# Kernel optimization log

Measured on AMD Instinct MI355X. Metric: run time of the kernel, lower is better.

## Reference

```python
import jax, jax.numpy as jnp
import numpy as np

B, N, D = 4, 2048, 1024
H, A, Lv = 8, 128, 128   # heads, attention_dim (qk), linear_dim (v)
NUM_BLOCKS = 4
QKV_W = (2 * Lv + 2 * A) * H  # 4096
NEG = -1e9


def setup_inputs() -> dict:
    key = jax.random.key(0)
    ks = jax.random.split(key, 10)
    past_lengths = jax.random.randint(ks[0], (B,), 0, N)
    past_ids = jax.random.randint(ks[1], (B, N), 0, 10000)
    past_embeddings = jax.random.normal(ks[2], (B, N, D), dtype=jnp.float32)
    # per-block parameters, stacked on leading block axis (xavier-ish scale)
    qkv_w = jax.random.normal(ks[3], (NUM_BLOCKS, D, QKV_W), dtype=jnp.float32) * (1.0 / np.sqrt(D))
    qkv_b = jnp.zeros((NUM_BLOCKS, QKV_W), dtype=jnp.float32)
    out_w = jax.random.normal(ks[4], (NUM_BLOCKS, Lv * H, D), dtype=jnp.float32) * (1.0 / np.sqrt(Lv * H))
    out_b = jnp.zeros((NUM_BLOCKS, D), dtype=jnp.float32)
    ln_g = jnp.ones((NUM_BLOCKS, D), dtype=jnp.float32)
    ln_b = jnp.zeros((NUM_BLOCKS, D), dtype=jnp.float32)
    return {"past_lengths": past_lengths, "past_ids": past_ids,
            "past_embeddings": past_embeddings, "qkv_w": qkv_w, "qkv_b": qkv_b,
            "out_w": out_w, "out_b": out_b, "ln_g": ln_g, "ln_b": ln_b}


def _layer_norm(x, g, b, eps=1e-5):
    mu = jnp.mean(x, axis=-1, keepdims=True)
    var = jnp.mean(jnp.square(x - mu), axis=-1, keepdims=True)
    return (x - mu) * jax.lax.rsqrt(var + eps) * g + b


def _block(x, mask, qw, qb, ow, ob, g, b):
    xn = _layer_norm(x, g, b)
    qkv = (xn @ qw + qb).reshape(B, N, H, 2 * Lv + 2 * A)
    q = qkv[..., :A]              # [B,N,H,A]
    k = qkv[..., A:2 * A]         # [B,N,H,A]
    v = qkv[..., 2 * A:2 * A + Lv]  # [B,N,H,Lv]
    scores = jnp.einsum('bnha,bmha->bhnm', q, k) / np.sqrt(A)
    # original: masked_fill(-inf) -> silu -> /N -> softmax; we mask after the
    # silu transform with a large-negative logit so masked weights are ~0
    logits = jnp.where(mask[:, None, :, :], jax.nn.silu(scores) / N, NEG)
    w = jax.nn.softmax(logits, axis=-1)
    attn = jnp.einsum('bhnm,bmhl->bnhl', w, v).reshape(B, N, H * Lv)
    return x + attn @ ow + ob


def reference(past_lengths, past_ids, past_embeddings, qkv_w, qkv_b, out_w, out_b, ln_g, ln_b):
    valid = past_ids != 0                                   # [B,N]
    causal = jnp.triu(jnp.ones((N, N), dtype=bool), k=1)     # faithful to buffer (triu, diag=1)
    mask = causal[None] & valid[:, None, :] & valid[:, :, None]  # [B,N,N]
    x = past_embeddings
    for i in range(NUM_BLOCKS):
        x = _block(x, mask, qkv_w[i], qkv_b[i], out_w[i], out_b[i], ln_g[i], ln_b[i])
    return x
```

## Files before the change

kernel.cpp:

```cpp
#include <hip/hip_runtime.h>

typedef __bf16 bf16_t;
typedef __bf16 bf16x8 __attribute__((ext_vector_type(8)));
typedef __bf16 bf16x4 __attribute__((ext_vector_type(4)));
typedef float f32x4 __attribute__((ext_vector_type(4)));

#define B_ 4
#define N_ 2048
#define D_ 1024
#define H_ 8
#define NB_ 4
#define M_ (B_*N_)
#define QN_ 3072
#define QKN_ 2048

__device__ __forceinline__ void async_copy16(const void* gsrc, void* ldst) {
    __builtin_amdgcn_global_load_lds(
        (const __attribute__((address_space(1))) void*)gsrc,
        (__attribute__((address_space(3))) void*)ldst, 16, 0, 0);
}

static constexpr size_t WT_OFF  = 0;
static constexpr size_t WT_SZ   = (size_t)NB_*QN_*D_*2;
static constexpr size_t OWT_OFF = WT_OFF + WT_SZ;
static constexpr size_t OWT_SZ  = (size_t)NB_*D_*D_*2;
static constexpr size_t XN_OFF  = OWT_OFF + OWT_SZ;
static constexpr size_t XN_SZ   = (size_t)M_*D_*2;
static constexpr size_t QK_OFF  = XN_OFF + XN_SZ;
static constexpr size_t QK_SZ   = (size_t)M_*QKN_*2;
static constexpr size_t VT_OFF  = QK_OFF + QK_SZ;
static constexpr size_t VT_SZ   = (size_t)32*128*N_*2;
static constexpr size_t ATT_OFF = VT_OFF + VT_SZ;
static constexpr size_t ATT_SZ  = (size_t)M_*D_*2;
static constexpr size_t QBR_OFF = ATT_OFF + ATT_SZ;
static constexpr size_t QBR_SZ  = (size_t)NB_*QN_*4;
static constexpr size_t VS_OFF  = QBR_OFF + QBR_SZ;

__global__ __launch_bounds__(256) void repack_qkvw(const float* __restrict__ qw, bf16_t* __restrict__ wt)
{
    __shared__ float tile[64][65];
    const int nb = blockIdx.z;
    const int j0 = blockIdx.x * 64, d0 = blockIdx.y * 64;
    const int tx = threadIdx.x, ty = threadIdx.y;
    const float* src = qw + (size_t)nb * D_ * 4096;
    const int jj = j0 + tx;
    const int sel = jj >> 10, rr = jj & 1023, hh = rr >> 7, aa = rr & 127;
    const int orig = hh * 512 + sel * 128 + aa;
#pragma unroll
    for (int it = 0; it < 16; ++it) {
        int dr = it * 4 + ty;
        tile[dr][tx] = src[(size_t)(d0 + dr) * 4096 + orig];
    }
    __syncthreads();
    bf16_t* dst = wt + (size_t)nb * QN_ * D_;
#pragma unroll
    for (int it = 0; it < 16; ++it) {
        int jr = it * 4 + ty;
        dst[(size_t)(j0 + jr) * D_ + d0 + tx] = (bf16_t)tile[tx][jr];
    }
}

__global__ __launch_bounds__(256) void repack_outw(const float* __restrict__ ow, bf16_t* __restrict__ owt)
{
    __shared__ float tile[64][65];
    const int nb = blockIdx.z;
    const int j0 = blockIdx.x * 64, d0 = blockIdx.y * 64;
    const int tx = threadIdx.x, ty = threadIdx.y;
    const float* src = ow + (size_t)nb * D_ * D_;
#pragma unroll
    for (int it = 0; it < 16; ++it) {
        int dr = it * 4 + ty;
        tile[dr][tx] = src[(size_t)(d0 + dr) * D_ + j0 + tx];
    }
    __syncthreads();
    bf16_t* dst = owt + (size_t)nb * D_ * D_;
#pragma unroll
    for (int it = 0; it < 16; ++it) {
        int jr = it * 4 + ty;
        dst[(size_t)(j0 + jr) * D_ + d0 + tx] = (bf16_t)tile[tx][jr];
    }
}

__global__ __launch_bounds__(256) void repack_qb(const float* __restrict__ qb, float* __restrict__ qbr)
{
    int idx = blockIdx.x * 256 + threadIdx.x;
    int nb = idx / QN_, jj = idx % QN_;
    int sel = jj >> 10, rr = jj & 1023, hh = rr >> 7, aa = rr & 127;
    qbr[idx] = qb[nb * 4096 + hh * 512 + sel * 128 + aa];
}

__global__ __launch_bounds__(256) void ln_kernel(const float* __restrict__ x, const float* __restrict__ g,
                                                 const float* __restrict__ bb, bf16_t* __restrict__ xn)
{
    const int row = blockIdx.x, tid = threadIdx.x;
    const float4 v = ((const float4*)(x + (size_t)row * D_))[tid];
    float s = v.x + v.y + v.z + v.w;
    float q = v.x * v.x + v.y * v.y + v.z * v.z + v.w * v.w;
#pragma unroll
    for (int d = 32; d >= 1; d >>= 1) { s += __shfl_xor(s, d); q += __shfl_xor(q, d); }
    __shared__ float ls[4], lq[4];
    if ((tid & 63) == 0) { ls[tid >> 6] = s; lq[tid >> 6] = q; }
    __syncthreads();
    s = ls[0] + ls[1] + ls[2] + ls[3];
    q = lq[0] + lq[1] + lq[2] + lq[3];
    const float mean = s * (1.f / 1024.f);
    const float var  = q * (1.f / 1024.f) - mean * mean;
    const float inv  = rsqrtf(var + 1e-5f);
    const float4 gg = ((const float4*)g)[tid];
    const float4 bv = ((const float4*)bb)[tid];
    bf16x4 o;
    o[0] = (bf16_t)((v.x - mean) * inv * gg.x + bv.x);
    o[1] = (bf16_t)((v.y - mean) * inv * gg.y + bv.y);
    o[2] = (bf16_t)((v.z - mean) * inv * gg.z + bv.z);
    o[3] = (bf16_t)((v.w - mean) * inv * gg.w + bv.w);
    *(bf16x4*)(xn + (size_t)row * D_ + tid * 4) = o;
}

__global__ __launch_bounds__(512, 2) void gemm_qkv(const bf16_t* __restrict__ Am, const bf16_t* __restrict__ Bt,
                                                   const float* __restrict__ bias,
                                                   bf16_t* __restrict__ outQK, bf16_t* __restrict__ vtOut)
{
    __shared__ bf16_t As[4 * 8192];
    __shared__ bf16_t Bs[4 * 6144];
    const int tid = threadIdx.x;
    const int lane = tid & 63, wave = tid >> 6;
    const int wr = wave >> 2, wc = wave & 3;
    const int quad = lane >> 4, l15 = lane & 15;
    const int swz = quad ^ ((l15 >> 1) & 3);
    const int slane8 = ((lane & 3) ^ ((lane >> 3) & 3)) * 8;
    const int lrow = lane >> 2;
    const int m0 = blockIdx.y * 256, n0 = blockIdx.x * 192;
    const int Kn = D_;
    const bool w4 = (wave < 4);

    const int ch = wave * 2;
    const int bch0 = w4 ? 2 * wave : 4 + wave;
    const int bch1 = w4 ? 2 * wave + 1 : bch0;
    const bf16_t* gA0 = Am + (size_t)(m0 + ch * 16 + lrow) * Kn + slane8;
    const bf16_t* gA1 = gA0 + (size_t)16 * Kn;
    const bf16_t* gB0 = Bt + (size_t)(n0 + bch0 * 16 + lrow) * Kn + slane8;
    const bf16_t* gB1 = Bt + (size_t)(n0 + bch1 * 16 + lrow) * Kn + slane8;
    bf16_t* const dA0 = &As[ch * 512 + lane * 8];
    bf16_t* const dA1 = &As[(ch + 1) * 512 + lane * 8];
    bf16_t* const dB0 = &Bs[bch0 * 512 + lane * 8];
    bf16_t* const dB1 = &Bs[bch1 * 512 + lane * 8];

    auto STAGE = [&](int slot) {
        async_copy16(gA0, dA0 + slot * 8192);
        async_copy16(gA1, dA1 + slot * 8192);
        async_copy16(gB0, dB0 + slot * 6144);
        if (w4) async_copy16(gB1, dB1 + slot * 6144);
        gA0 += 32; gA1 += 32; gB0 += 32; gB1 += 32;
    };

    f32x4 acc[8][3] = {};
    const int NT = Kn >> 5;

    STAGE(0); STAGE(1); STAGE(2);
    if (w4) asm volatile("s_waitcnt vmcnt(8)" ::: "memory");
    else    asm volatile("s_waitcnt vmcnt(6)" ::: "memory");
    __builtin_amdgcn_s_barrier();

    const int aoff = wr * 4096 + l15 * 32 + swz * 8;
    const int boff = wc * 1536 + l15 * 32 + swz * 8;

    for (int t = 0; t < NT; ++t) {
        const int ring = t & 3;
        const bf16_t* ra = &As[ring * 8192 + aoff];
        const bf16_t* rb = &Bs[ring * 6144 + boff];
        bf16x8 af[8], bfv[3];
#pragma unroll
        for (int j = 0; j < 3; ++j) bfv[j] = *(const bf16x8*)(rb + j * 512);
#pragma unroll
        for (int i = 0; i < 8; ++i) af[i] = *(const bf16x8*)(ra + i * 512);
        if (t + 3 < NT) STAGE((t + 3) & 3);
        __builtin_amdgcn_s_setprio(1);
#pragma unroll
        for (int i = 0; i < 8; ++i)
#pragma unroll
            for (int j = 0; j < 3; ++j)
                acc[i][j] = __builtin_amdgcn_mfma_f32_16x16x32_bf16(af[i], bfv[j], acc[i][j], 0, 0, 0);
        __builtin_amdgcn_s_setprio(0);
        if (t + 3 < NT) {
            if (w4) asm volatile("s_waitcnt vmcnt(8)" ::: "memory");
            else    asm volatile("s_waitcnt vmcnt(6)" ::: "memory");
        } else if (t + 2 < NT) {
            if (w4) asm volatile("s_waitcnt vmcnt(4)" ::: "memory");
            else    asm volatile("s_waitcnt vmcnt(3)" ::: "memory");
        } else if (t + 1 < NT) {
            asm volatile("s_waitcnt vmcnt(0)" ::: "memory");
        }
        __builtin_amdgcn_s_barrier();
    }

#pragma unroll
    for (int i = 0; i < 8; ++i) {
        const int rowg = m0 + wr * 128 + i * 16 + quad * 4;
        const int bb2 = rowg >> 11, mloc = rowg & 2047;
        const int mperm = (mloc & ~31) | (((mloc >> 2) & 3) << 3) | (((mloc >> 4) & 1) << 2);
#pragma unroll
        for (int j = 0; j < 3; ++j) {
            const int colg = n0 + wc * 48 + j * 16 + l15;
            const float bv = bias[colg];
            if (colg >= 2048) {
                const int hh = (colg - 2048) >> 7, ll = (colg - 2048) & 127;
                bf16x4 sv;
#pragma unroll
                for (int r = 0; r < 4; ++r) sv[r] = (bf16_t)(acc[i][j][r] + bv);
                *(bf16x4*)(vtOut + ((size_t)(bb2 * 8 + hh) * 128 + ll) * (size_t)N_ + mperm) = sv;
            } else {
#pragma unroll
                for (int r = 0; r < 4; ++r)
                    outQK[(size_t)(rowg + r) * QKN_ + colg] = (bf16_t)(acc[i][j][r] + bv);
            }
        }
    }
}

template<bool RESID>
__global__ __launch_bounds__(512, 2) void gemm256(const bf16_t* __restrict__ Am, const bf16_t* __restrict__ Bt,
                                                  const float* __restrict__ bias, float* __restrict__ resid_out,
                                                  bf16_t* __restrict__ outH, bf16_t* __restrict__ vtOut,
                                                  int Kn, int Nn, int vSplit)
{
    __shared__ bf16_t As[4 * 256 * 32];
    __shared__ bf16_t Bs[4 * 128 * 32];
    const int tid = threadIdx.x;
    const int lane = tid & 63, wave = tid >> 6;
    const int wr = wave >> 2, wc = wave & 3;
    const int quad = lane >> 4, l15 = lane & 15;
    const int swz = quad ^ ((l15 >> 1) & 3);
    const int slane8 = ((lane & 3) ^ ((lane >> 3) & 3)) * 8;
    const int lrow = lane >> 2;
    const int m0 = blockIdx.y * 256, n0 = blockIdx.x * 128;

    const int chA0 = wave * 2, chA1 = chA0 + 1;
    const bf16_t* gA0 = Am + (size_t)(m0 + chA0 * 16 + lrow) * Kn + slane8;
    const bf16_t* gA1 = Am + (size_t)(m0 + chA1 * 16 + lrow) * Kn + slane8;
    const bf16_t* gB  = Bt + (size_t)(n0 + wave * 16 + lrow) * Kn + slane8;
    bf16_t* const dA0 = &As[chA0 * 512];
    bf16_t* const dA1 = &As[chA1 * 512];
    bf16_t* const dB  = &Bs[wave * 512];

    auto STAGE = [&](int slot) {
        async_copy16(gA0, dA0 + slot * 8192);
        async_copy16(gA1, dA1 + slot * 8192);
        async_copy16(gB,  dB  + slot * 4096);
        gA0 += 32; gA1 += 32; gB += 32;
    };

    f32x4 acc[8][2] = {};
    const int NT = Kn >> 5;

    STAGE(0); STAGE(1); STAGE(2);
    asm volatile("s_waitcnt vmcnt(6)" ::: "memory");
    __builtin_amdgcn_s_barrier();

    const int aoff = (wr * 128 + l15) * 32 + swz * 8;
    const int boff = (wc * 32  + l15) * 32 + swz * 8;

    for (int t = 0; t < NT; ++t) {
        const int ring = t & 3;
        const bf16_t* ra = &As[ring * 8192 + aoff];
        const bf16_t* rb = &Bs[ring * 4096 + boff];
        bf16x8 af[8], bfv[2];
#pragma unroll
        for (int i = 0; i < 8; ++i) af[i] = *(const bf16x8*)(ra + i * 512);
#pragma unroll
        for (int j = 0; j < 2; ++j) bfv[j] = *(const bf16x8*)(rb + j * 512);
        if (t + 3 < NT) STAGE((t + 3) & 3);
        __builtin_amdgcn_s_barrier();
        asm volatile("s_waitcnt lgkmcnt(0)" ::: "memory");
        __builtin_amdgcn_s_setprio(1);
#pragma unroll
        for (int i = 0; i < 8; ++i)
#pragma unroll
            for (int j = 0; j < 2; ++j)
                acc[i][j] = __builtin_amdgcn_mfma_f32_16x16x32_bf16(af[i], bfv[j], acc[i][j], 0, 0, 0);
        __builtin_amdgcn_s_setprio(0);
        if (t + 3 < NT)      asm volatile("s_waitcnt vmcnt(6)" ::: "memory");
        else if (t + 2 < NT) asm volatile("s_waitcnt vmcnt(3)" ::: "memory");
        else if (t + 1 < NT) asm volatile("s_waitcnt vmcnt(0)" ::: "memory");
        __builtin_amdgcn_s_barrier();
    }

    if (!RESID && n0 >= vSplit) {
#pragma unroll
        for (int i = 0; i < 8; ++i) {
            const int rowg = m0 + wr * 128 + i * 16 + quad * 4;
            const int bb2 = rowg >> 11, mloc = rowg & 2047;
            const int mperm = (mloc & ~31) | (((mloc >> 2) & 3) << 3) | (((mloc >> 4) & 1) << 2);
#pragma unroll
            for (int j = 0; j < 2; ++j) {
                const int colg = n0 + wc * 32 + j * 16 + l15;
                const int hh = (colg - 2048) >> 7, ll = (colg - 2048) & 127;
                const float bv = bias[colg];
                bf16x4 sv;
#pragma unroll
                for (int r = 0; r < 4; ++r) sv[r] = (bf16_t)(acc[i][j][r] + bv);
                *(bf16x4*)(vtOut + ((size_t)(bb2 * 8 + hh) * 128 + ll) * (size_t)N_ + mperm) = sv;
            }
        }
        return;
    }
#pragma unroll
    for (int i = 0; i < 8; ++i) {
#pragma unroll
        for (int j = 0; j < 2; ++j) {
            const int colg = n0 + wc * 32 + j * 16 + l15;
            const float bv = bias[colg];
#pragma unroll
            for (int r = 0; r < 4; ++r) {
                const int rowg = m0 + wr * 128 + i * 16 + quad * 4 + r;
                const size_t off = (size_t)rowg * Nn + colg;
                const float v = acc[i][j][r] + bv;
                if (RESID) resid_out[off] += v;
                else       outH[off] = (bf16_t)v;
            }
        }
    }
}

__global__ __launch_bounds__(256) void vsum_kernel(const bf16_t* __restrict__ vt, float* __restrict__ vs)
{
    const int gid = blockIdx.x * 4 + (threadIdx.x >> 6);
    const int lane = threadIdx.x & 63;
    const bf16_t* p = vt + (size_t)gid * N_ + lane * 8;
    float s = 0.f;
#pragma unroll
    for (int c = 0; c < 4; ++c) {
        bf16x8 v = *(const bf16x8*)(p + c * 512);
#pragma unroll
        for (int u = 0; u < 8; ++u) s += (float)v[u];
    }
#pragma unroll
    for (int d = 32; d >= 1; d >>= 1) s += __shfl_xor(s, d);
    if (lane == 0) vs[gid] = s;
}

template<bool CAUSAL>
__device__ __forceinline__ void attn_tile(
    int m0, int m0n, int n0, int b, int h,
    const bf16_t* __restrict__ qk, const bf16_t* __restrict__ vtb,
    bf16_t* Ks, bf16_t* Vs, const unsigned int* mb,
    const bf16x8 (&qf)[2][4], bf16x8 onesf, float vnf0, float vnf1,
    f32x4 (&oacc)[2][8], f32x4 (&dacc)[2])
{
    const int tid = threadIdx.x, lane = tid & 63, wave = tid >> 6;
    const int quad = lane >> 4, l15 = lane & 15;
    const int swz = quad ^ ((l15 >> 1) & 3);
    const int slane8 = ((lane & 3) ^ ((lane >> 3) & 3)) * 8;
    const int lrow = lane >> 2;
    const float scaleA = 0.08838834764831845f;
    const float invN = 1.f / 2048.f;

#pragma unroll
    for (int s = 0; s < 8; ++s) {
        const int kkc = s & 3, rg = (s >> 2) + wave * 2;
        async_copy16(vtb + (size_t)(rg * 16 + lrow) * N_ + m0 + kkc * 32 + slane8,
                     &Vs[kkc * 4096 + rg * 512 + lane * 8]);
    }

    f32x4 sacc[2][8] = {};
    __builtin_amdgcn_s_setprio(1);
#pragma unroll
    for (int kk = 0; kk < 4; ++kk) {
#pragma unroll
        for (int j = 0; j < 8; ++j) {
            bf16x8 kf = *(const bf16x8*)&Ks[kk * 4096 + (j * 16 + l15) * 32 + swz * 8];
            sacc[0][j] = __builtin_amdgcn_mfma_f32_16x16x32_bf16(kf, qf[0][kk], sacc[0][j], 0, 0, 0);
            sacc[1][j] = __builtin_amdgcn_mfma_f32_16x16x32_bf16(kf, qf[1][kk], sacc[1][j], 0, 0, 0);
        }
    }
    __builtin_amdgcn_s_setprio(0);

    unsigned int wj[4];
#pragma unroll
    for (int q = 0; q < 4; ++q) wj[q] = mb[(m0 >> 5) + q];
    bf16x8 pf[2][4];
#pragma unroll
    for (int kk = 0; kk < 4; ++kk) {
#pragma unroll
        for (int s = 0; s < 2; ++s) {
            const int j = kk * 2 + s;
            const unsigned int wrd = wj[j >> 1];
            const int shl = (j & 1) * 16 + quad * 4;
#pragma unroll
            for (int nb = 0; nb < 2; ++nb) {
                const float vn = nb ? vnf1 : vnf0;
#pragma unroll
                for (int r = 0; r < 4; ++r) {
                    const float sv = sacc[nb][j][r] * scaleA;
                    const float xc = fminf(fmaxf(sv, -4.f), 4.f);
                    float sig = __builtin_fmaf(xc, 0.25f, 0.5f);
                    sig = __builtin_fmaf(-(xc * 0.03125f), fabsf(xc), sig);
                    float e = __builtin_fmaf(sv * sig, invN, 1.f);
                    e = ((wrd >> (shl + r)) & 1) ? e * vn : 0.f;
                    if (CAUSAL) {
                        const int dmn = (m0 + j * 16 + quad * 4 + r) - (n0 + wave * 32 + nb * 16 + l15);
                        e = (dmn > 0) ? e : 0.f;
                    }
                    pf[nb][kk][s * 4 + r] = (bf16_t)e;
                }
            }
        }
    }

    __syncthreads();

    if (m0n < N_) {
        const size_t baseq = (size_t)b * N_ * QKN_;
#pragma unroll
        for (int s = 0; s < 8; ++s) {
            const int kkc = s & 3, rg = (s >> 2) + wave * 2;
            async_copy16(qk + baseq + (size_t)(m0n + rg * 16 + lrow) * QKN_ + 1024 + h * 128 + kkc * 32 + slane8,
                         &Ks[kkc * 4096 + rg * 512 + lane * 8]);
        }
    }

    __builtin_amdgcn_s_setprio(1);
#pragma unroll
    for (int kk = 0; kk < 4; ++kk) {
        dacc[0] = __builtin_amdgcn_mfma_f32_16x16x32_bf16(pf[0][kk], onesf, dacc[0], 0, 0, 0);
        dacc[1] = __builtin_amdgcn_mfma_f32_16x16x32_bf16(pf[1][kk], onesf, dacc[1], 0, 0, 0);
#pragma unroll
        for (int j = 0; j < 8; ++j) {
            bf16x8 vf = *(const bf16x8*)&Vs[kk * 4096 + (j * 16 + l15) * 32 + swz * 8];
            oacc[0][j] = __builtin_amdgcn_mfma_f32_16x16x32_bf16(pf[0][kk], vf, oacc[0][j], 0, 0, 0);
            oacc[1][j] = __builtin_amdgcn_mfma_f32_16x16x32_bf16(pf[1][kk], vf, oacc[1][j], 0, 0, 0);
        }
    }
    __builtin_amdgcn_s_setprio(0);
    __syncthreads();
}

__global__ __launch_bounds__(256, 2) void attn_kernel(const bf16_t* __restrict__ qk, const bf16_t* __restrict__ vt,
                                                      const int* __restrict__ past_ids, const float* __restrict__ vsum,
                                                      bf16_t* __restrict__ att)
{
    __shared__ bf16_t Ks[4 * 128 * 32];
    __shared__ bf16_t Vs[4 * 128 * 32];
    __shared__ unsigned long long mbits[32];

    const int bx = blockIdx.x;
    const int bh = bx & 31, g = bx >> 5;
    const int t = (g < 8) ? g : 23 - g;
    const int b = bh >> 3, h = bh & 7;
    const int n0 = t << 7;
    const int tid = threadIdx.x, lane = tid & 63, wave = tid >> 6;
    const int quad = lane >> 4, l15 = lane & 15;
    const int slane8 = ((lane & 3) ^ ((lane >> 3) & 3)) * 8;
    const int lrow = lane >> 2;
    const bf16_t* vtb = vt + (size_t)bh * 128 * N_;
    const float invN = 1.f / 2048.f;

#pragma unroll
    for (int it = 0; it < 8; ++it) {
        const int m = (wave * 8 + it) * 64 + lane;
        const unsigned long long bal = __ballot(past_ids[b * N_ + m] != 0);
        if (lane == 0) mbits[wave * 8 + it] = bal;
    }

    bf16x8 qf[2][4];
#pragma unroll
    for (int nb = 0; nb < 2; ++nb) {
        const bf16_t* gq = qk + (size_t)b * N_ * QKN_ + (size_t)(n0 + wave * 32 + nb * 16 + l15) * QKN_ + h * 128 + quad * 8;
#pragma unroll
        for (int kk = 0; kk < 4; ++kk) qf[nb][kk] = *(const bf16x8*)(gq + kk * 32);
    }
    const float vnf0 = past_ids[b * N_ + n0 + wave * 32 + l15] != 0 ? 1.f : 0.f;
    const float vnf1 = past_ids[b * N_ + n0 + wave * 32 + 16 + l15] != 0 ? 1.f : 0.f;
    bf16x8 onesf;
#pragma unroll
    for (int i = 0; i < 8; ++i) onesf[i] = (bf16_t)1.f;

    {
        const size_t baseq = (size_t)b * N_ * QKN_;
#pragma unroll
        for (int s = 0; s < 8; ++s) {
            const int kkc = s & 3, rg = (s >> 2) + wave * 2;
            async_copy16(qk + baseq + (size_t)(n0 + rg * 16 + lrow) * QKN_ + 1024 + h * 128 + kkc * 32 + slane8,
                         &Ks[kkc * 4096 + rg * 512 + lane * 8]);
        }
    }
    __syncthreads();

    f32x4 oacc[2][8] = {};
    f32x4 dacc[2] = {};
    const unsigned int* mb = (const unsigned int*)mbits;

    attn_tile<true>(n0, n0 + 128, n0, b, h, qk, vtb, Ks, Vs, mb, qf, onesf, vnf0, vnf1, oacc, dacc);
    for (int m0 = n0 + 128; m0 < N_; m0 += 128)
        attn_tile<false>(m0, m0 + 128, n0, b, h, qk, vtb, Ks, Vs, mb, qf, onesf, vnf0, vnf1, oacc, dacc);

    float vsr[8];
#pragma unroll
    for (int j = 0; j < 8; ++j) vsr[j] = vsum[bh * 128 + j * 16 + l15];
#pragma unroll
    for (int nb = 0; nb < 2; ++nb) {
#pragma unroll
        for (int r = 0; r < 4; ++r) {
            const float dn = dacc[nb][r];
            const bool uni = !(dn > 0.f);
            const float rc = uni ? 0.f : __builtin_amdgcn_rcpf(dn);
            const int gn = n0 + wave * 32 + nb * 16 + quad * 4 + r;
#pragma unroll
            for (int j = 0; j < 8; ++j) {
                const float ov = uni ? (vsr[j] * invN) : (oacc[nb][j][r] * rc);
                att[(size_t)(b * N_ + gn) * 1024 + h * 128 + j * 16 + l15] = (bf16_t)ov;
            }
        }
    }
}

extern "C" void kernel_launch(void* const* d_in, const int* in_sizes, int n_in,
                              void* d_out, int out_size, void* d_ws, size_t ws_size,
                              hipStream_t stream) {
    (void)in_sizes; (void)n_in; (void)out_size; (void)ws_size;
    const int*   past_ids = (const int*)d_in[1];
    const float* past_emb = (const float*)d_in[2];
    const float* qkv_w    = (const float*)d_in[3];
    const float* qkv_b    = (const float*)d_in[4];
    const float* out_w    = (const float*)d_in[5];
    const float* out_b    = (const float*)d_in[6];
    const float* ln_g     = (const float*)d_in[7];
    const float* ln_b     = (const float*)d_in[8];

    float* x = (float*)d_out;
    char* ws = (char*)d_ws;
    bf16_t* WT  = (bf16_t*)(ws + WT_OFF);
    bf16_t* OWT = (bf16_t*)(ws + OWT_OFF);
    bf16_t* XN  = (bf16_t*)(ws + XN_OFF);
    bf16_t* QK  = (bf16_t*)(ws + QK_OFF);
    bf16_t* VT  = (bf16_t*)(ws + VT_OFF);
    bf16_t* ATT = (bf16_t*)(ws + ATT_OFF);
    float*  QBR = (float*)(ws + QBR_OFF);
    float*  VS  = (float*)(ws + VS_OFF);

    hipMemcpyAsync(x, past_emb, (size_t)M_ * D_ * sizeof(float), hipMemcpyDeviceToDevice, stream);
    repack_qkvw<<<dim3(48, 16, NB_), dim3(64, 4), 0, stream>>>(qkv_w, WT);
    repack_outw<<<dim3(16, 16, NB_), dim3(64, 4), 0, stream>>>(out_w, OWT);
    repack_qb<<<48, 256, 0, stream>>>(qkv_b, QBR);

    for (int layer = 0; layer < NB_; ++layer) {
        ln_kernel<<<M_, 256, 0, stream>>>(x, ln_g + layer * D_, ln_b + layer * D_, XN);
        gemm_qkv<<<dim3(QN_ / 192, M_ / 256), 512, 0, stream>>>(
            XN, WT + (size_t)layer * QN_ * D_, QBR + layer * QN_, QK, VT);
        vsum_kernel<<<1024, 256, 0, stream>>>(VT, VS);
        attn_kernel<<<512, 256, 0, stream>>>(QK, VT, past_ids, VS, ATT);
        gemm256<true><<<dim3(D_ / 128, M_ / 256), 512, 0, stream>>>(
            ATT, OWT + (size_t)layer * D_ * D_, out_b + layer * D_, x, nullptr, nullptr, D_, D_, 1 << 30);
    }
}
```

Before: 876.2 us.

## Precompute key-validity bitmask in bf16 layout and fold scales out of attention inner loop

Moves the 1/sqrt(A) scale into the QKV GEMM epilogue, folds the 1/N factor into the sigmoid polynomial constants, and replaces per-element bit extraction with a precomputed per-key 16-bit mask that is ANDed onto packed bf16 probabilities. Query-row validity is now applied only at the final normalization instead of per element. The aim is fewer VALU ops in the attention softmax path and removal of the per-block ballot setup. It adds a small mask kernel, extra global mask loads per tile, and rounds the pre-scaled Q to bf16, which shifts numerics slightly.

```diff
diff --git a/kernel.cpp b/kernel.cpp
--- a/kernel.cpp
+++ b/kernel.cpp
@@ -4,6 +4,7 @@
 typedef __bf16 bf16x8 __attribute__((ext_vector_type(8)));
 typedef __bf16 bf16x4 __attribute__((ext_vector_type(4)));
 typedef float f32x4 __attribute__((ext_vector_type(4)));
+typedef unsigned int u32x4 __attribute__((ext_vector_type(4)));
 
 #define B_ 4
 #define N_ 2048
@@ -35,6 +36,8 @@
 static constexpr size_t QBR_OFF = ATT_OFF + ATT_SZ;
 static constexpr size_t QBR_SZ  = (size_t)NB_*QN_*4;
 static constexpr size_t VS_OFF  = QBR_OFF + QBR_SZ;
+static constexpr size_t VS_SZ   = (size_t)32*128*4;
+static constexpr size_t MASK_OFF = VS_OFF + VS_SZ;
 
 __global__ __launch_bounds__(256) void repack_qkvw(const float* __restrict__ qw, bf16_t* __restrict__ wt)
 {
@@ -87,6 +90,15 @@
     int nb = idx / QN_, jj = idx % QN_;
     int sel = jj >> 10, rr = jj & 1023, hh = rr >> 7, aa = rr & 127;
     qbr[idx] = qb[nb * 4096 + hh * 512 + sel * 128 + aa];
+}
+
+__global__ __launch_bounds__(256) void mask_kernel(const int* __restrict__ past_ids, unsigned short* __restrict__ maskA)
+{
+    const int idx = blockIdx.x * 256 + threadIdx.x;
+    const int b = idx >> 11, P = idx & 2047;
+    const int k = P & 31;
+    const int m = (P & ~31) | (((k >> 2) & 1) << 4) | (((k >> 3) & 3) << 2) | (k & 3);
+    maskA[idx] = past_ids[b * N_ + m] != 0 ? 0xFFFFu : 0u;
 }
 
 __global__ __launch_bounds__(256) void ln_kernel(const float* __restrict__ x, const float* __restrict__ g,
@@ -209,9 +221,10 @@
                 for (int r = 0; r < 4; ++r) sv[r] = (bf16_t)(acc[i][j][r] + bv);
                 *(bf16x4*)(vtOut + ((size_t)(bb2 * 8 + hh) * 128 + ll) * (size_t)N_ + mperm) = sv;
             } else {
+                const float qs = (colg < 1024) ? 0.08838834764831845f : 1.f;
 #pragma unroll
                 for (int r = 0; r < 4; ++r)
-                    outQK[(size_t)(rowg + r) * QKN_ + colg] = (bf16_t)(acc[i][j][r] + bv);
+                    outQK[(size_t)(rowg + r) * QKN_ + colg] = (bf16_t)((acc[i][j][r] + bv) * qs);
             }
         }
     }
@@ -342,8 +355,9 @@
 __device__ __forceinline__ void attn_tile(
     int m0, int m0n, int n0, int b, int h,
     const bf16_t* __restrict__ qk, const bf16_t* __restrict__ vtb,
-    bf16_t* Ks, bf16_t* Vs, const unsigned int* mb,
-    const bf16x8 (&qf)[2][4], bf16x8 onesf, float vnf0, float vnf1,
+    const unsigned short* __restrict__ maskB,
+    bf16_t* Ks, bf16_t* Vs,
+    const bf16x8 (&qf)[2][4], bf16x8 onesf,
     f32x4 (&oacc)[2][8], f32x4 (&dacc)[2])
 {
     const int tid = threadIdx.x, lane = tid & 63, wave = tid >> 6;
@@ -351,7 +365,6 @@
     const int swz = quad ^ ((l15 >> 1) & 3);
     const int slane8 = ((lane & 3) ^ ((lane >> 3) & 3)) * 8;
     const int lrow = lane >> 2;
-    const float scaleA = 0.08838834764831845f;
     const float invN = 1.f / 2048.f;
 
 #pragma unroll
@@ -360,6 +373,10 @@
         async_copy16(vtb + (size_t)(rg * 16 + lrow) * N_ + m0 + kkc * 32 + slane8,
                      &Vs[kkc * 4096 + rg * 512 + lane * 8]);
     }
+    bf16x8 mAf[4];
+#pragma unroll
+    for (int kk = 0; kk < 4; ++kk)
+        mAf[kk] = *(const bf16x8*)(maskB + m0 + kk * 32 + quad * 8);
 
     f32x4 sacc[2][8] = {};
     __builtin_amdgcn_s_setprio(1);
@@ -374,28 +391,21 @@
     }
     __builtin_amdgcn_s_setprio(0);
 
-    unsigned int wj[4];
-#pragma unroll
-    for (int q = 0; q < 4; ++q) wj[q] = mb[(m0 >> 5) + q];
     bf16x8 pf[2][4];
 #pragma unroll
     for (int kk = 0; kk < 4; ++kk) {
 #pragma unroll
         for (int s = 0; s < 2; ++s) {
             const int j = kk * 2 + s;
-            const unsigned int wrd = wj[j >> 1];
-            const int shl = (j & 1) * 16 + quad * 4;
 #pragma unroll
             for (int nb = 0; nb < 2; ++nb) {
-                const float vn = nb ? vnf1 : vnf0;
 #pragma unroll
                 for (int r = 0; r < 4; ++r) {
-                    const float sv = sacc[nb][j][r] * scaleA;
-                    const float xc = fminf(fmaxf(sv, -4.f), 4.f);
-                    float sig = __builtin_fmaf(xc, 0.25f, 0.5f);
-                    sig = __builtin_fmaf(-(xc * 0.03125f), fabsf(xc), sig);
-                    float e = __builtin_fmaf(sv * sig, invN, 1.f);
-                    e = ((wrd >> (shl + r)) & 1) ? e * vn : 0.f;
+                    const float sv = sacc[nb][j][r];
+                    const float xc = __builtin_amdgcn_fmed3f(sv, -4.f, 4.f);
+                    float sg = __builtin_fmaf(xc, 0.25f * invN, 0.5f * invN);
+                    sg = __builtin_fmaf(-(xc * (0.03125f * invN)), fabsf(xc), sg);
+                    float e = __builtin_fmaf(sv, sg, 1.f);
                     if (CAUSAL) {
                         const int dmn = (m0 + j * 16 + quad * 4 + r) - (n0 + wave * 32 + nb * 16 + l15);
                         e = (dmn > 0) ? e : 0.f;
@@ -404,6 +414,8 @@
                 }
             }
         }
+        *(u32x4*)&pf[0][kk] = *(u32x4*)&pf[0][kk] & *(const u32x4*)&mAf[kk];
+        *(u32x4*)&pf[1][kk] = *(u32x4*)&pf[1][kk] & *(const u32x4*)&mAf[kk];
     }
 
     __syncthreads();
@@ -436,11 +448,11 @@
 
 __global__ __launch_bounds__(256, 2) void attn_kernel(const bf16_t* __restrict__ qk, const bf16_t* __restrict__ vt,
                                                       const int* __restrict__ past_ids, const float* __restrict__ vsum,
+                                                      const unsigned short* __restrict__ maskA,
                                                       bf16_t* __restrict__ att)
 {
     __shared__ bf16_t Ks[4 * 128 * 32];
     __shared__ bf16_t Vs[4 * 128 * 32];
-    __shared__ unsigned long long mbits[32];
 
     const int bx = blockIdx.x;
     const int bh = bx & 31, g = bx >> 5;
@@ -452,14 +464,8 @@
     const int slane8 = ((lane & 3) ^ ((lane >> 3) & 3)) * 8;
     const int lrow = lane >> 2;
     const bf16_t* vtb = vt + (size_t)bh * 128 * N_;
+    const unsigned short* maskB = maskA + b * N_;
     const float invN = 1.f / 2048.f;
-
-#pragma unroll
-    for (int it = 0; it < 8; ++it) {
-        const int m = (wave * 8 + it) * 64 + lane;
-        const unsigned long long bal = __ballot(past_ids[b * N_ + m] != 0);
-        if (lane == 0) mbits[wave * 8 + it] = bal;
-    }
 
     bf16x8 qf[2][4];
 #pragma unroll
@@ -487,21 +493,21 @@
 
     f32x4 oacc[2][8] = {};
     f32x4 dacc[2] = {};
-    const unsigned int* mb = (const unsigned int*)mbits;
-
-    attn_tile<true>(n0, n0 + 128, n0, b, h, qk, vtb, Ks, Vs, mb, qf, onesf, vnf0, vnf1, oacc, dacc);
+
+    attn_tile<true>(n0, n0 + 128, n0, b, h, qk, vtb, maskB, Ks, Vs, qf, onesf, oacc, dacc);
     for (int m0 = n0 + 128; m0 < N_; m0 += 128)
-        attn_tile<false>(m0, m0 + 128, n0, b, h, qk, vtb, Ks, Vs, mb, qf, onesf, vnf0, vnf1, oacc, dacc);
+        attn_tile<false>(m0, m0 + 128, n0, b, h, qk, vtb, maskB, Ks, Vs, qf, onesf, oacc, dacc);
 
     float vsr[8];
 #pragma unroll
     for (int j = 0; j < 8; ++j) vsr[j] = vsum[bh * 128 + j * 16 + l15];
 #pragma unroll
     for (int nb = 0; nb < 2; ++nb) {
+        const float vn = nb ? vnf1 : vnf0;
 #pragma unroll
         for (int r = 0; r < 4; ++r) {
             const float dn = dacc[nb][r];
-            const bool uni = !(dn > 0.f);
+            const bool uni = (vn == 0.f) || !(dn > 0.f);
             const float rc = uni ? 0.f : __builtin_amdgcn_rcpf(dn);
             const int gn = n0 + wave * 32 + nb * 16 + quad * 4 + r;
 #pragma unroll
@@ -536,18 +542,20 @@
     bf16_t* ATT = (bf16_t*)(ws + ATT_OFF);
     float*  QBR = (float*)(ws + QBR_OFF);
     float*  VS  = (float*)(ws + VS_OFF);
+    unsigned short* MASKA = (unsigned short*)(ws + MASK_OFF);
 
     hipMemcpyAsync(x, past_emb, (size_t)M_ * D_ * sizeof(float), hipMemcpyDeviceToDevice, stream);
     repack_qkvw<<<dim3(48, 16, NB_), dim3(64, 4), 0, stream>>>(qkv_w, WT);
     repack_outw<<<dim3(16, 16, NB_), dim3(64, 4), 0, stream>>>(out_w, OWT);
     repack_qb<<<48, 256, 0, stream>>>(qkv_b, QBR);
+    mask_kernel<<<32, 256, 0, stream>>>(past_ids, MASKA);
 
     for (int layer = 0; layer < NB_; ++layer) {
         ln_kernel<<<M_, 256, 0, stream>>>(x, ln_g + layer * D_, ln_b + layer * D_, XN);
         gemm_qkv<<<dim3(QN_ / 192, M_ / 256), 512, 0, stream>>>(
             XN, WT + (size_t)layer * QN_ * D_, QBR + layer * QN_, QK, VT);
         vsum_kernel<<<1024, 256, 0, stream>>>(VT, VS);
-        attn_kernel<<<512, 256, 0, stream>>>(QK, VT, past_ids, VS, ATT);
+        attn_kernel<<<512, 256, 0, stream>>>(QK, VT, past_ids, VS, MASKA, ATT);
         gemm256<true><<<dim3(D_ / 128, M_ / 256), 512, 0, stream>>>(
             ATT, OWT + (size_t)layer * D_ * D_, out_b + layer * D_, x, nullptr, nullptr, D_, D_, 1 << 30);
     }
```

After: 868.6 us. About the same (-0.9%).
